# Performance work log

Hardware: AMD Instinct MI355X
Metric: run time of the kernel (lower is better)

The kernel has to match this reference:

```python
import jax, jax.numpy as jnp
import numpy as np

# ---- static config (matches init_kwargs) ----
B, S, D = 2, 4096, 1024          # batch, seq_len, dim_input
L, ST = 512, 64                  # segment_len, state_len
H = 8                            # num_heads
DK0, DV0, DK1, DV1 = 64, 64, 64, 64  # per-head key/value dims for 2 memory levels
DH = 4096                        # dim_hidden (MLP)
T = 2 * ST + L                   # tokens per segment block: [state, segment, state]


def setup_inputs() -> dict:
    key = jax.random.key(0)
    ks = jax.random.split(key, 18)
    f32 = jnp.float32
    def w(k, shape, fan_in):
        return (jax.random.normal(k, shape, dtype=f32) / np.float32(np.sqrt(fan_in)))
    return {
        "x": jax.random.normal(ks[0], (B, S, D), dtype=f32),
        "state_init": 0.02 * jax.random.normal(ks[1], (ST, D), dtype=f32),
        # level-0 projections: dim_input -> per-head (key/value)
        "Wq0": w(ks[2], (D, H, DK0), D),
        "Wk0": w(ks[3], (D, H, DK0), D),
        "Wv0": w(ks[4], (D, H, DV0), D),
        # level-1 projections: level-0 value dim -> per-head (key/value)
        "Wq1": w(ks[5], (H, DV0, DK1), DV0),
        "Wk1": w(ks[6], (H, DV0, DK1), DV0),
        "Wv1": w(ks[7], (H, DV0, DV1), DV0),
        # output projection back to dim_input
        "Wo": w(ks[8], (H, DV1, D), H * DV1),
        "bo": jnp.zeros((D,), f32),
        "g_attn": jnp.ones((D,), f32),
        "b_attn": jnp.zeros((D,), f32),
        "W1": w(ks[9], (D, DH), D),
        "b1": jnp.zeros((DH,), f32),
        "W2": w(ks[10], (DH, D), DH),
        "b2": jnp.zeros((D,), f32),
        "g_mlp": jnp.ones((D,), f32),
        "b_mlp": jnp.zeros((D,), f32),
    }


def _layernorm(x, g, b, eps=1e-5):
    mu = jnp.mean(x, axis=-1, keepdims=True)
    var = jnp.mean(jnp.square(x - mu), axis=-1, keepdims=True)
    return (x - mu) * jax.lax.rsqrt(var + eps) * g + b


def _rope(x, pos):
    # x: (B, H, T, dk); rotary embedding with base 10000
    dk = x.shape[-1]
    inv_freq = jnp.power(jnp.float32(10000.0), -jnp.arange(0, dk, 2, dtype=jnp.float32) / dk)
    ang = pos[:, None] * inv_freq[None, :]              # (T, dk/2)
    cos, sin = jnp.cos(ang), jnp.sin(ang)
    x1, x2 = x[..., 0::2], x[..., 1::2]
    r1 = x1 * cos - x2 * sin
    r2 = x1 * sin + x2 * cos
    return jnp.stack([r1, r2], axis=-1).reshape(x.shape)


def _attend(q, k, v, mask):
    # q,k: (B,H,T,dk); v: (B,H,T,dv); causal mask (T,T)
    scale = jnp.float32(1.0 / np.sqrt(q.shape[-1]))
    scores = jnp.einsum('bhqc,bhkc->bhqk', q, k) * scale
    scores = jnp.where(mask, scores, jnp.float32(-1e30))
    p = jax.nn.softmax(scores, axis=-1)
    return jnp.einsum('bhqk,bhkv->bhqv', p, v)


def _remmtas(x, state_init, Wq0, Wk0, Wv0, Wq1, Wk1, Wv1, Wo, bo):
    b, s, d = x.shape
    n_seg = s // L
    xs = x.reshape(b, n_seg, L, d).transpose(1, 0, 2, 3)   # (n_seg, B, L, D)
    mask = jnp.tril(jnp.ones((T, T), dtype=bool))
    pos = jnp.arange(T, dtype=jnp.float32)
    state0 = jnp.broadcast_to(state_init, (b, ST, d))

    def step(state, seg):
        toks = jnp.concatenate([state, seg, state], axis=1)      # (B, T, D)
        # memory level 0
        q0 = _rope(jnp.einsum('btd,dhk->bhtk', toks, Wq0), pos)
        k0 = _rope(jnp.einsum('btd,dhk->bhtk', toks, Wk0), pos)
        v0 = jnp.einsum('btd,dhv->bhtv', toks, Wv0)
        o0 = _attend(q0, k0, v0, mask)                           # (B,H,T,DV0)
        # memory level 1 (consumes level-0 values, per-head)
        q1 = _rope(jnp.einsum('bhtv,hvk->bhtk', o0, Wq1), pos)
        k1 = _rope(jnp.einsum('bhtv,hvk->bhtk', o0, Wk1), pos)
        v1 = jnp.einsum('bhtv,hvw->bhtw', o0, Wv1)
        o1 = _attend(q1, k1, v1, mask)                           # (B,H,T,DV1)
        out = jnp.einsum('bhtv,hvd->btd', o1, Wo) + bo           # (B,T,D)
        new_state = out[:, ST + L:]                              # trailing state tokens
        return new_state, out[:, ST:ST + L]                      # segment output

    _, outs = jax.lax.scan(step, state0, xs)                     # (n_seg, B, L, D)
    return outs.transpose(1, 0, 2, 3).reshape(b, s, d)


def reference(x, state_init, Wq0, Wk0, Wv0, Wq1, Wk1, Wv1, Wo, bo,
              g_attn, b_attn, W1, b1, W2, b2, g_mlp, b_mlp):
    a = _remmtas(x, state_init, Wq0, Wk0, Wv0, Wq1, Wk1, Wv1, Wo, bo)
    h = _layernorm(a + x, g_attn, b_attn)
    m = jax.nn.gelu(h @ W1 + b1, approximate=False) @ W2 + b2
    # note: second residual adds the ORIGINAL x, per the source code
    return _layernorm(m + x, g_mlp, b_mlp)
```

## Files before the change

kernel.cpp:

```cpp
#include <hip/hip_runtime.h>
#include <hip/hip_bf16.h>

typedef __hip_bfloat16 bf16;
typedef short bf16x8 __attribute__((ext_vector_type(8)));
typedef float f32x4 __attribute__((ext_vector_type(4)));

#define CB 2
#define CS 4096
#define CD 1024
#define CL 512
#define CST 64
#define CH 8
#define CT 640
#define CDH 4096
#define NSEG 8
#define LP 80

__device__ __forceinline__ float tof(float x) { return x; }
__device__ __forceinline__ float tof(bf16 x) { return __bfloat162float(x); }
__device__ __forceinline__ void storev(float* p, float v) { *p = v; }
__device__ __forceinline__ void storev(bf16* p, float v) { *p = __float2bfloat16(v); }

__device__ __forceinline__ float ldin(const void* p, size_t i, int f32w) {
    if (f32w) return ((const float*)p)[i];
    return __bfloat162float(((const bf16*)p)[i]);
}

__global__ void sniff_kernel(const void* x, int* flag) {
    if (threadIdx.x == 0 && blockIdx.x == 0) {
        const bf16* hb = (const bf16*)x;
        int plaus = 0;
        for (int i = 0; i < 256; ++i) {
            float v = __bfloat162float(hb[2 * i]);
            float a = fabsf(v);
            if (v == 0.f || (a > 1e-4f && a < 100.f)) ++plaus;
        }
        flag[0] = (plaus < 128) ? 1 : 0;
    }
}

__global__ __launch_bounds__(256) void transpose_kernel(
    const void* __restrict__ in, bf16* __restrict__ out, int R, int C,
    const int* __restrict__ flag)
{
    const int f32w = flag[0];
    __shared__ short t[64][72];
    int tid = threadIdx.x;
    int c0 = blockIdx.x * 64, r0 = blockIdx.y * 64;
    int cc = tid & 63, rr = tid >> 6;
#pragma unroll
    for (int i = 0; i < 16; ++i) {
        bf16 v = __float2bfloat16(ldin(in, (size_t)(r0 + rr + i * 4) * C + c0 + cc, f32w));
        t[rr + i * 4][cc] = *(short*)&v;
    }
    __syncthreads();
#pragma unroll
    for (int i = 0; i < 16; ++i)
        ((short*)out)[(size_t)(c0 + rr + i * 4) * R + r0 + cc] = t[cc][rr + i * 4];
}

__global__ __launch_bounds__(256) void transpose3_kernel(
    const void* __restrict__ in0, const void* __restrict__ in1, const void* __restrict__ in2,
    bf16* __restrict__ out0, bf16* __restrict__ out1, bf16* __restrict__ out2,
    const int* __restrict__ flag)
{
    const int f32w = flag[0];
    const void* in = (blockIdx.z == 0) ? in0 : (blockIdx.z == 1 ? in1 : in2);
    bf16* out = (blockIdx.z == 0) ? out0 : (blockIdx.z == 1 ? out1 : out2);
    const int R = CD, C = 512;
    __shared__ short t[64][72];
    int tid = threadIdx.x;
    int c0 = blockIdx.x * 64, r0 = blockIdx.y * 64;
    int cc = tid & 63, rr = tid >> 6;
#pragma unroll
    for (int i = 0; i < 16; ++i) {
        bf16 v = __float2bfloat16(ldin(in, (size_t)(r0 + rr + i * 4) * C + c0 + cc, f32w));
        t[rr + i * 4][cc] = *(short*)&v;
    }
    __syncthreads();
#pragma unroll
    for (int i = 0; i < 16; ++i)
        ((short*)out)[(size_t)(c0 + rr + i * 4) * R + r0 + cc] = t[cc][rr + i * 4];
}

__global__ __launch_bounds__(256) void transposeH_kernel(
    const void* __restrict__ Wq1, const void* __restrict__ Wk1, const void* __restrict__ Wv1,
    bf16* __restrict__ oq, bf16* __restrict__ ok, bf16* __restrict__ ov,
    const int* __restrict__ flag)
{
    const int f32w = flag[0];
    int which = blockIdx.x >> 3, hh = blockIdx.x & 7;
    const void* in = (which == 0) ? Wq1 : (which == 1) ? Wk1 : Wv1;
    bf16* out = (which == 0) ? oq : (which == 1) ? ok : ov;
    __shared__ short t[64][72];
    int tid = threadIdx.x;
    int cc = tid & 63, rr = tid >> 6;
    size_t base = (size_t)hh * 4096;
#pragma unroll
    for (int i = 0; i < 16; ++i) {
        bf16 v = __float2bfloat16(ldin(in, base + (size_t)(rr + i * 4) * 64 + cc, f32w));
        t[rr + i * 4][cc] = *(short*)&v;
    }
    __syncthreads();
#pragma unroll
    for (int i = 0; i < 16; ++i)
        ((short*)out)[base + (size_t)(rr + i * 4) * 64 + cc] = t[cc][rr + i * 4];
}

template <typename TC, int ACT, int OUTM, int ACCUM>
__global__ __launch_bounds__(256) void mfma_lds(
    const bf16* __restrict__ A,
    const bf16* __restrict__ Bt0, const bf16* __restrict__ Bt1, const bf16* __restrict__ Bt2,
    TC* __restrict__ C0, TC* __restrict__ C1, TC* __restrict__ C2,
    const void* __restrict__ bias, int boff,
    int M, int N, int K, int lda, int ldb, int seg,
    const int* __restrict__ flag)
{
    const int f32w = flag[0];
    const bf16* Bt = (blockIdx.z == 0) ? Bt0 : (blockIdx.z == 1 ? Bt1 : Bt2);
    TC* C = (blockIdx.z == 0) ? C0 : (blockIdx.z == 1 ? C1 : C2);

    __shared__ __align__(16) short As[128 * 64];
    __shared__ __align__(16) short Bs[128 * 64];

    const int tid = threadIdx.x;
    const int lane = tid & 63;
    const int w = tid >> 6;
    const int wm = w >> 1, wn = w & 1;
    const int bm = blockIdx.x * 128, bn = blockIdx.y * 128;

    f32x4 acc[4][4];
#pragma unroll
    for (int i = 0; i < 4; ++i)
#pragma unroll
        for (int j = 0; j < 4; ++j) acc[i][j] = (f32x4){0.f, 0.f, 0.f, 0.f};

    int srow[4], skc[4];
#pragma unroll
    for (int i = 0; i < 4; ++i) {
        int c = i * 256 + tid;
        srow[i] = c >> 3;
        skc[i] = (c & 7) * 8;
    }

    bf16x8 rA0[4], rB0[4], rA1[4], rB1[4];
#pragma unroll
    for (int i = 0; i < 4; ++i) {
        rA0[i] = *(const bf16x8*)(A + (size_t)(bm + srow[i]) * lda + skc[i]);
        rB0[i] = *(const bf16x8*)(Bt + (size_t)(bn + srow[i]) * ldb + skc[i]);
        rA1[i] = *(const bf16x8*)(A + (size_t)(bm + srow[i]) * lda + 64 + skc[i]);
        rB1[i] = *(const bf16x8*)(Bt + (size_t)(bn + srow[i]) * ldb + 64 + skc[i]);
    }

#define MFMA_PHASE                                                              \
    _Pragma("unroll")                                                           \
    for (int kh = 0; kh < 2; ++kh) {                                            \
        bf16x8 av[4], bv[4];                                                    \
        _Pragma("unroll")                                                       \
        for (int mi = 0; mi < 4; ++mi) {                                        \
            int r = wm * 64 + mi * 16 + (lane & 15);                            \
            int cl = kh * 4 + (lane >> 4);                                      \
            av[mi] = *(const bf16x8*)&As[r * 64 + cl * 8];                      \
        }                                                                       \
        _Pragma("unroll")                                                       \
        for (int nj = 0; nj < 4; ++nj) {                                        \
            int r = wn * 64 + nj * 16 + (lane & 15);                            \
            int cl = kh * 4 + (lane >> 4);                                      \
            bv[nj] = *(const bf16x8*)&Bs[r * 64 + cl * 8];                      \
        }                                                                       \
        _Pragma("unroll")                                                       \
        for (int mi = 0; mi < 4; ++mi)                                          \
            _Pragma("unroll")                                                   \
            for (int nj = 0; nj < 4; ++nj)                                      \
                acc[mi][nj] = __builtin_amdgcn_mfma_f32_16x16x32_bf16(          \
                    av[mi], bv[nj], acc[mi][nj], 0, 0, 0);                      \
    }

    for (int k0 = 0; k0 < K; k0 += 128) {
        __syncthreads();
#pragma unroll
        for (int i = 0; i < 4; ++i) {
            *(bf16x8*)&As[(size_t)(i * 256 + tid) * 8] = rA0[i];
            *(bf16x8*)&Bs[(size_t)(i * 256 + tid) * 8] = rB0[i];
        }
        if (k0 + 128 < K) {
            int kn = k0 + 128;
#pragma unroll
            for (int i = 0; i < 4; ++i) {
                rA0[i] = *(const bf16x8*)(A + (size_t)(bm + srow[i]) * lda + kn + skc[i]);
                rB0[i] = *(const bf16x8*)(Bt + (size_t)(bn + srow[i]) * ldb + kn + skc[i]);
            }
        }
        __syncthreads();
        MFMA_PHASE

        __syncthreads();
#pragma unroll
        for (int i = 0; i < 4; ++i) {
            *(bf16x8*)&As[(size_t)(i * 256 + tid) * 8] = rA1[i];
            *(bf16x8*)&Bs[(size_t)(i * 256 + tid) * 8] = rB1[i];
        }
        if (k0 + 192 < K) {
            int kn = k0 + 192;
#pragma unroll
            for (int i = 0; i < 4; ++i) {
                rA1[i] = *(const bf16x8*)(A + (size_t)(bm + srow[i]) * lda + kn + skc[i]);
                rB1[i] = *(const bf16x8*)(Bt + (size_t)(bn + srow[i]) * ldb + kn + skc[i]);
            }
        }
        __syncthreads();
        MFMA_PHASE
    }
#undef MFMA_PHASE

#pragma unroll
    for (int mi = 0; mi < 4; ++mi) {
#pragma unroll
        for (int nj = 0; nj < 4; ++nj) {
            int c = bn + wn * 64 + nj * 16 + (lane & 15);
            float bia = bias ? ldin(bias, boff + c, f32w) : 0.f;
#pragma unroll
            for (int r = 0; r < 4; ++r) {
                int row = bm + wm * 64 + mi * 16 + (lane >> 4) * 4 + r;
                float v = acc[mi][nj][r] + bia;
                if (ACT == 1) v = 0.5f * v * (1.0f + erff(v * 0.70710678118654752f));
                if (OUTM == 0) {
                    if (ACCUM) v += tof(C[(size_t)row * N + c]);
                    storev(C + (size_t)row * N + c, v);
                } else {
                    int bb2 = row / CT, t = row % CT;
                    if (t >= CST) {
                        if (t < CST + CL)
                            storev(C0 + ((size_t)bb2 * CS + (size_t)seg * CL + (t - CST)) * CD + c, v);
                        else
                            storev(C1 + ((size_t)bb2 * CST + (t - CST - CL)) * CD + c, v);
                    }
                }
            }
        }
    }
}

__global__ __launch_bounds__(256) void ropeV_kernel(
    bf16* __restrict__ q, bf16* __restrict__ k,
    const bf16* __restrict__ v, bf16* __restrict__ vt)
{
    int t0 = blockIdx.x * 64, hh = blockIdx.y, b = blockIdx.z;
    int tid = threadIdx.x;
    __shared__ short lt[64][72];
    int c = tid & 63;
    int r0 = tid >> 6;
    int ip = c >> 1;
    float inv = powf(10000.f, -(float)(2 * ip) / 64.f);
#pragma unroll
    for (int i = 0; i < 16; ++i) {
        int r = r0 + i * 4;
        int t = t0 + r;
        size_t idx = ((size_t)b * CT + t) * 512 + hh * 64 + c;
        float qv = tof(q[idx]);
        float kv = tof(k[idx]);
        float ang = (float)t * inv;
        float sn, cs;
        sincosf(ang, &sn, &cs);
        float qp = __shfl_xor(qv, 1);
        float kp = __shfl_xor(kv, 1);
        float rq, rk;
        if (c & 1) { rq = qp * sn + qv * cs; rk = kp * sn + kv * cs; }
        else       { rq = qv * cs - qp * sn; rk = kv * cs - kp * sn; }
        q[idx] = __float2bfloat16(rq);
        k[idx] = __float2bfloat16(rk);
        lt[r][c] = ((const short*)v)[idx];
    }
    __syncthreads();
#pragma unroll
    for (int i = 0; i < 16; ++i) {
        int c2 = r0 + i * 4;
        int r2 = c;
        ((short*)vt)[((size_t)(b * CH + hh) * 64 + c2) * CT + t0 + r2] = lt[r2][c2];
    }
}

template <int FUSE>
__global__ __launch_bounds__(256) void attn_mfma(
    const bf16* __restrict__ q, const bf16* __restrict__ k, const bf16* __restrict__ vt,
    bf16* __restrict__ o,
    int qsb, int qsh, int qst,
    int ksb, int ksh, int kst,
    int ob, int oh, int ot,
    const bf16* __restrict__ Wq1t, const bf16* __restrict__ Wk1t, const bf16* __restrict__ Wv1t,
    bf16* __restrict__ q1o, bf16* __restrict__ k1o, bf16* __restrict__ v1to)
{
    const int tid = threadIdx.x;
    const int lane = tid & 63;
    const int wrow = tid >> 6;
    const int hh = blockIdx.y, b = blockIdx.z;
    const int qbase = ((int)gridDim.x - 1 - (int)blockIdx.x) * 64;

    __shared__ __align__(16) short Qs[64 * LP];
    __shared__ __align__(16) short Ks[64 * LP];
    __shared__ __align__(16) short Vs[64 * LP];
    __shared__ __align__(16) short Ps[64 * LP];

    const size_t qb0 = (size_t)b * qsb + (size_t)hh * qsh;
    const size_t kb0 = (size_t)b * ksb + (size_t)hh * ksh;
    const size_t vtb = (size_t)(b * CH + hh) * 64 * CT;

    int srow[2], skc[2], soff[2];
#pragma unroll
    for (int i = 0; i < 2; ++i) {
        int c = i * 256 + tid;
        srow[i] = c >> 3;
        skc[i] = c & 7;
        soff[i] = srow[i] * LP + skc[i] * 8;
    }

    bf16x8 rQ[2], rK[2], rV[2];
#pragma unroll
    for (int i = 0; i < 2; ++i) {
        rQ[i] = *(const bf16x8*)(q + qb0 + (size_t)(qbase + srow[i]) * qst + skc[i] * 8);
        rK[i] = *(const bf16x8*)(k + kb0 + (size_t)srow[i] * kst + skc[i] * 8);
        rV[i] = *(const bf16x8*)(vt + vtb + (size_t)srow[i] * CT + skc[i] * 8);
    }

    float mrow[4], lrow[4];
    f32x4 oacc[4];
#pragma unroll
    for (int r = 0; r < 4; ++r) { mrow[r] = -1e30f; lrow[r] = 0.f; }
#pragma unroll
    for (int nd = 0; nd < 4; ++nd) oacc[nd] = (f32x4){0.f, 0.f, 0.f, 0.f};

    const int ntiles = qbase / 64 + 1;
    for (int ti = 0; ti < ntiles; ++ti) {
        __syncthreads();
        if (ti == 0) {
#pragma unroll
            for (int i = 0; i < 2; ++i) *(bf16x8*)&Qs[soff[i]] = rQ[i];
        }
#pragma unroll
        for (int i = 0; i < 2; ++i) {
            *(bf16x8*)&Ks[soff[i]] = rK[i];
            *(bf16x8*)&Vs[soff[i]] = rV[i];
        }
        if (ti + 1 < ntiles) {
            int j1 = (ti + 1) * 64;
#pragma unroll
            for (int i = 0; i < 2; ++i) {
                rK[i] = *(const bf16x8*)(k + kb0 + (size_t)(j1 + srow[i]) * kst + skc[i] * 8);
                rV[i] = *(const bf16x8*)(vt + vtb + (size_t)srow[i] * CT + j1 + skc[i] * 8);
            }
        }
        __syncthreads();

        f32x4 sacc[4];
#pragma unroll
        for (int nj = 0; nj < 4; ++nj) sacc[nj] = (f32x4){0.f, 0.f, 0.f, 0.f};
#pragma unroll
        for (int kh = 0; kh < 2; ++kh) {
            int cl = kh * 4 + (lane >> 4);
            bf16x8 av = *(const bf16x8*)&Qs[(wrow * 16 + (lane & 15)) * LP + cl * 8];
#pragma unroll
            for (int nj = 0; nj < 4; ++nj) {
                bf16x8 bv = *(const bf16x8*)&Ks[(nj * 16 + (lane & 15)) * LP + cl * 8];
                sacc[nj] = __builtin_amdgcn_mfma_f32_16x16x32_bf16(av, bv, sacc[nj], 0, 0, 0);
            }
        }

        const bool diag = (ti == ntiles - 1);
        float pm[4] = {-1e30f, -1e30f, -1e30f, -1e30f};
#pragma unroll
        for (int nj = 0; nj < 4; ++nj) {
            int col_l = nj * 16 + (lane & 15);
#pragma unroll
            for (int r = 0; r < 4; ++r) {
                int row_l = wrow * 16 + ((lane >> 4) << 2) + r;
                float s = (diag && col_l > row_l) ? -1e30f : sacc[nj][r] * 0.125f;
                sacc[nj][r] = s;
                pm[r] = fmaxf(pm[r], s);
            }
        }
#pragma unroll
        for (int msk = 1; msk < 16; msk <<= 1)
#pragma unroll
            for (int r = 0; r < 4; ++r) pm[r] = fmaxf(pm[r], __shfl_xor(pm[r], msk));

        float corr[4], rs[4] = {0.f, 0.f, 0.f, 0.f};
#pragma unroll
        for (int r = 0; r < 4; ++r) {
            float mn = fmaxf(mrow[r], pm[r]);
            corr[r] = __expf(mrow[r] - mn);
            mrow[r] = mn;
        }
#pragma unroll
        for (int nj = 0; nj < 4; ++nj)
#pragma unroll
            for (int r = 0; r < 4; ++r) {
                float p = __expf(sacc[nj][r] - mrow[r]);
                sacc[nj][r] = p;
                rs[r] += p;
            }
#pragma unroll
        for (int msk = 1; msk < 16; msk <<= 1)
#pragma unroll
            for (int r = 0; r < 4; ++r) rs[r] += __shfl_xor(rs[r], msk);
#pragma unroll
        for (int r = 0; r < 4; ++r) lrow[r] = lrow[r] * corr[r] + rs[r];
#pragma unroll
        for (int nd = 0; nd < 4; ++nd)
#pragma unroll
            for (int r = 0; r < 4; ++r) oacc[nd][r] *= corr[r];

#pragma unroll
        for (int nj = 0; nj < 4; ++nj)
#pragma unroll
            for (int r = 0; r < 4; ++r) {
                bf16 pb = __float2bfloat16(sacc[nj][r]);
                Ps[(wrow * 16 + ((lane >> 4) << 2) + r) * LP + nj * 16 + (lane & 15)] =
                    *(short*)&pb;
            }

#pragma unroll
        for (int kh = 0; kh < 2; ++kh) {
            int cl = kh * 4 + (lane >> 4);
            bf16x8 pa = *(const bf16x8*)&Ps[(wrow * 16 + (lane & 15)) * LP + cl * 8];
#pragma unroll
            for (int nd = 0; nd < 4; ++nd) {
                bf16x8 bv = *(const bf16x8*)&Vs[(nd * 16 + (lane & 15)) * LP + cl * 8];
                oacc[nd] = __builtin_amdgcn_mfma_f32_16x16x32_bf16(pa, bv, oacc[nd], 0, 0, 0);
            }
        }
    }

    if (FUSE == 0) {
#pragma unroll
        for (int nd = 0; nd < 4; ++nd) {
#pragma unroll
            for (int r = 0; r < 4; ++r) {
                int row_g = qbase + wrow * 16 + ((lane >> 4) << 2) + r;
                int col = nd * 16 + (lane & 15);
                storev(&o[(size_t)b * ob + (size_t)hh * oh + (size_t)row_g * ot + col],
                       oacc[nd][r] / lrow[r]);
            }
        }
    } else {
#pragma unroll
        for (int nd = 0; nd < 4; ++nd)
#pragma unroll
            for (int r = 0; r < 4; ++r) {
                int row_l = wrow * 16 + ((lane >> 4) << 2) + r;
                bf16 ob16 = __float2bfloat16(oacc[nd][r] / lrow[r]);
                Qs[row_l * LP + nd * 16 + (lane & 15)] = *(short*)&ob16;
            }
        __syncthreads();

        const size_t whb = (size_t)hh * 4096;
        f32x4 qa[4], ka[4], va[4];
#pragma unroll
        for (int nj = 0; nj < 4; ++nj) {
            qa[nj] = (f32x4){0.f, 0.f, 0.f, 0.f};
            ka[nj] = (f32x4){0.f, 0.f, 0.f, 0.f};
            va[nj] = (f32x4){0.f, 0.f, 0.f, 0.f};
        }
#pragma unroll
        for (int kh = 0; kh < 2; ++kh) {
            int cl = kh * 4 + (lane >> 4);
            bf16x8 av = *(const bf16x8*)&Qs[(wrow * 16 + (lane & 15)) * LP + cl * 8];
#pragma unroll
            for (int nj = 0; nj < 4; ++nj) {
                int rowb = nj * 16 + (lane & 15);
                bf16x8 bq = *(const bf16x8*)(Wq1t + whb + (size_t)rowb * 64 + cl * 8);
                bf16x8 bk = *(const bf16x8*)(Wk1t + whb + (size_t)rowb * 64 + cl * 8);
                bf16x8 bw = *(const bf16x8*)(Wv1t + whb + (size_t)rowb * 64 + cl * 8);
                qa[nj] = __builtin_amdgcn_mfma_f32_16x16x32_bf16(av, bq, qa[nj], 0, 0, 0);
                ka[nj] = __builtin_amdgcn_mfma_f32_16x16x32_bf16(av, bk, ka[nj], 0, 0, 0);
                va[nj] = __builtin_amdgcn_mfma_f32_16x16x32_bf16(av, bw, va[nj], 0, 0, 0);
            }
        }
        const size_t bh = (size_t)(b * CH + hh);
#pragma unroll
        for (int nj = 0; nj < 4; ++nj) {
            int col = nj * 16 + (lane & 15);
            int ip = col >> 1;
            float inv = powf(10000.f, -(float)(2 * ip) / 64.f);
#pragma unroll
            for (int r = 0; r < 4; ++r) {
                int row_l = wrow * 16 + ((lane >> 4) << 2) + r;
                int t = qbase + row_l;
                float ang = (float)t * inv;
                float sn, cs;
                sincosf(ang, &sn, &cs);
                float aq = qa[nj][r], ak = ka[nj][r];
                float pq = __shfl_xor(aq, 1);
                float pk = __shfl_xor(ak, 1);
                float rq, rk;
                if (col & 1) { rq = pq * sn + aq * cs; rk = pk * sn + ak * cs; }
                else         { rq = aq * cs - pq * sn; rk = ak * cs - pk * sn; }
                size_t roff = (bh * CT + t) * 64 + col;
                q1o[roff] = __float2bfloat16(rq);
                k1o[roff] = __float2bfloat16(rk);
                v1to[(bh * 64 + col) * CT + t] = __float2bfloat16(va[nj][r]);
            }
        }
    }
}

__global__ __launch_bounds__(256) void build_toks_kernel(
    const void* __restrict__ x, const float* __restrict__ state, bf16* __restrict__ toks,
    int seg, const int* __restrict__ flag)
{
    const int f32w = flag[0];
    int idx = blockIdx.x * 256 + threadIdx.x;
    int d = idx & (CD - 1);
    int t = (idx >> 10) % CT;
    int b = idx / (CT * CD);
    float v;
    if (t < CST) v = state[(b * CST + t) * CD + d];
    else if (t < CST + CL) v = ldin(x, ((size_t)b * CS + seg * CL + (t - CST)) * CD + d, f32w);
    else v = state[(b * CST + (t - CST - CL)) * CD + d];
    toks[idx] = __float2bfloat16(v);
}

__global__ __launch_bounds__(256) void init_state_kernel(
    const void* __restrict__ s0, float* __restrict__ state, const int* __restrict__ flag)
{
    const int f32w = flag[0];
    int idx = blockIdx.x * 256 + threadIdx.x;
    state[idx] = ldin(s0, idx % (CST * CD), f32w);
}

__global__ __launch_bounds__(256) void ln_kernel(
    const float* __restrict__ ra, const void* __restrict__ x,
    const void* __restrict__ g, const void* __restrict__ bb,
    void* __restrict__ outp, int out_ext, const int* __restrict__ flag)
{
    const int f32w = flag[0];
    int row = blockIdx.x;
    int tid = threadIdx.x;
    __shared__ float buf[CD];
    __shared__ float red[4];

    float s = 0.f;
    for (int c = tid; c < CD; c += 256) {
        float v = ra[(size_t)row * CD + c] + ldin(x, (size_t)row * CD + c, f32w);
        buf[c] = v;
        s += v;
    }
#pragma unroll
    for (int off = 32; off; off >>= 1) s += __shfl_xor(s, off);
    if ((tid & 63) == 0) red[tid >> 6] = s;
    __syncthreads();
    float mu = (red[0] + red[1] + red[2] + red[3]) * (1.f / CD);
    __syncthreads();

    float vs = 0.f;
    for (int c = tid; c < CD; c += 256) {
        float d0 = buf[c] - mu;
        vs += d0 * d0;
    }
#pragma unroll
    for (int off = 32; off; off >>= 1) vs += __shfl_xor(vs, off);
    if ((tid & 63) == 0) red[tid >> 6] = vs;
    __syncthreads();
    float var = (red[0] + red[1] + red[2] + red[3]) * (1.f / CD);
    float rs = rsqrtf(var + 1e-5f);

    for (int c = tid; c < CD; c += 256) {
        float y = (buf[c] - mu) * rs * ldin(g, c, f32w) + ldin(bb, c, f32w);
        size_t idx = (size_t)row * CD + c;
        if (!out_ext) {
            ((bf16*)outp)[idx] = __float2bfloat16(y);
        } else if (f32w) {
            ((float*)outp)[idx] = y;
        } else {
            ((bf16*)outp)[idx] = __float2bfloat16(y);
        }
    }
}

extern "C" void kernel_launch(void* const* d_in, const int* in_sizes, int n_in,
                              void* d_out, int out_size, void* d_ws, size_t ws_size,
                              hipStream_t stream)
{
    const void* x      = d_in[0];
    const void* s0     = d_in[1];
    const void* Wq0    = d_in[2];
    const void* Wk0    = d_in[3];
    const void* Wv0    = d_in[4];
    const void* Wq1    = d_in[5];
    const void* Wk1    = d_in[6];
    const void* Wv1    = d_in[7];
    const void* Wo     = d_in[8];
    const void* bo     = d_in[9];
    const void* g_attn = d_in[10];
    const void* b_attn = d_in[11];
    const void* W1     = d_in[12];
    const void* b1     = d_in[13];
    const void* W2     = d_in[14];
    const void* b2     = d_in[15];
    const void* g_mlp  = d_in[16];
    const void* b_mlp  = d_in[17];

    int* flag = (int*)d_ws;
    float* f = (float*)((char*)d_ws + 16);
    float* toks_slot = f; f += (size_t)CB * CT * CD;
    float* q0_slot = f;  f += (size_t)CB * CH * CT * 64;
    float* k0_slot = f;  f += (size_t)CB * CH * CT * 64;
    float* v0_slot = f;  f += (size_t)CB * CH * CT * 64;
    float* o0_slot = f;  f += (size_t)CB * CH * CT * 64;
    float* q1_slot = f;  f += (size_t)CB * CH * CT * 64;
    float* k1_slot = f;  f += (size_t)CB * CH * CT * 64;
    float* v1_slot = f;  f += (size_t)CB * CH * CT * 64;
    float* o1t_slot = f; f += (size_t)CB * CT * (CH * 64);
    float* seg_slot = f; f += (size_t)CB * CT * CD;
    float* state = f;   f += (size_t)CB * CST * CD;
    float* a = f;       f += (size_t)CB * CS * CD;
    bf16* h = (bf16*)f;
    bf16* tail = h + (size_t)CB * CS * CD;

    bf16* toks = (bf16*)toks_slot;
    bf16* q0b = (bf16*)q0_slot;
    bf16* k0b = (bf16*)k0_slot;
    bf16* v0b = (bf16*)v0_slot;
    bf16* v0t = (bf16*)o0_slot;
    bf16* q1b = (bf16*)q1_slot;
    bf16* k1b = (bf16*)k1_slot;
    bf16* v1t = (bf16*)v1_slot;
    bf16* o1t = (bf16*)o1t_slot;
    bf16* WtQ = h;
    bf16* WtK = WtQ + (size_t)512 * 1024;
    bf16* WtV = WtK + (size_t)512 * 1024;
    bf16* WtO = WtV + (size_t)512 * 1024;
    bf16* WtQ1 = WtO + (size_t)1024 * 512;
    bf16* WtK1 = WtQ1 + (size_t)8 * 4096;
    bf16* WtV1 = WtK1 + (size_t)8 * 4096;
    bf16* g1  = (bf16*)toks_slot;
    bf16* Wt1 = g1 + (size_t)CB * CS * CD;
    bf16* Wt2 = tail;

    sniff_kernel<<<1, 64, 0, stream>>>(x, flag);
    init_state_kernel<<<(CB * CST * CD) / 256, 256, 0, stream>>>(s0, state, flag);

    transpose3_kernel<<<dim3(8, 16, 3), 256, 0, stream>>>(
        Wq0, Wk0, Wv0, WtQ, WtK, WtV, flag);
    transpose_kernel<<<dim3(16, 8), 256, 0, stream>>>(Wo, WtO, 512, CD, flag);
    transposeH_kernel<<<24, 256, 0, stream>>>(Wq1, Wk1, Wv1, WtQ1, WtK1, WtV1, flag);

    for (int seg = 0; seg < NSEG; ++seg) {
        build_toks_kernel<<<(CB * CT * CD) / 256, 256, 0, stream>>>(x, state, toks, seg, flag);
        mfma_lds<bf16, 0, 0, 0><<<dim3(10, 4, 3), 256, 0, stream>>>(
            toks, WtQ, WtK, WtV, q0b, k0b, v0b, nullptr, 0,
            CB * CT, 512, CD, CD, CD, 0, flag);
        ropeV_kernel<<<dim3(CT / 64, CH, CB), 256, 0, stream>>>(q0b, k0b, v0b, v0t);
        attn_mfma<1><<<dim3(CT / 64, CH, CB), 256, 0, stream>>>(
            q0b, k0b, v0t, nullptr,
            CT * 512, 64, 512,
            CT * 512, 64, 512,
            0, 0, 0,
            WtQ1, WtK1, WtV1, q1b, k1b, v1t);
        attn_mfma<0><<<dim3(CT / 64, CH, CB), 256, 0, stream>>>(
            q1b, k1b, v1t, o1t,
            CH * CT * 64, CT * 64, 64,
            CH * CT * 64, CT * 64, 64,
            CT * 512, 64, 512,
            nullptr, nullptr, nullptr, nullptr, nullptr, nullptr);
        mfma_lds<float, 0, 1, 0><<<dim3(10, 8, 1), 256, 0, stream>>>(
            o1t, WtO, WtO, WtO, a, state, a, bo, 0,
            CB * CT, CD, 512, 512, 512, seg, flag);
    }

    ln_kernel<<<CB * CS, 256, 0, stream>>>(a, x, g_attn, b_attn, h, 0, flag);

    transpose_kernel<<<dim3(CDH / 64, CD / 64), 256, 0, stream>>>(W1, Wt1, CD, CDH, flag);
    transpose_kernel<<<dim3(CD / 64, CDH / 64), 256, 0, stream>>>(W2, Wt2, CDH, CD, flag);

    for (int c = 0; c < 4; ++c) {
        mfma_lds<bf16, 1, 0, 0><<<dim3(64, 8, 1), 256, 0, stream>>>(
            h, Wt1 + (size_t)c * 1024 * CD, Wt1, Wt1, g1, g1, g1,
            b1, c * 1024, CB * CS, 1024, CD, CD, CD, 0, flag);
        if (c == 0)
            mfma_lds<float, 0, 0, 0><<<dim3(64, 8, 1), 256, 0, stream>>>(
                g1, Wt2 + (size_t)c * 1024, Wt2, Wt2, a, a, a,
                b2, 0, CB * CS, CD, 1024, 1024, CDH, 0, flag);
        else
            mfma_lds<float, 0, 0, 1><<<dim3(64, 8, 1), 256, 0, stream>>>(
                g1, Wt2 + (size_t)c * 1024, Wt2, Wt2, a, a, a,
                nullptr, 0, CB * CS, CD, 1024, 1024, CDH, 0, flag);
    }
    ln_kernel<<<CB * CS, 256, 0, stream>>>(a, x, g_mlp, b_mlp, d_out, 1, flag);
}
```

Measured before the change: 1.214 ms.

## Defer segment output projection to one batched GEMM after the scan

Inside the segment loop, the level-1 attention now skips the leading state query block. It writes segment rows to a staging buffer and the trailing state rows to a small buffer. Only the 128 state rows get the per-segment output projection, which keeps the recurrent state chain intact. The projection of all segment tokens is then done in one large GEMM over B*S rows after the loop, replacing eight small under-occupied GEMMs. This adds a new output-mode branch and extra bf16 scratch buffers carved from the workspace.

```diff
diff --git a/kernel.cpp b/kernel.cpp
--- a/kernel.cpp
+++ b/kernel.cpp
@@ -228,13 +228,7 @@
                     if (ACCUM) v += tof(C[(size_t)row * N + c]);
                     storev(C + (size_t)row * N + c, v);
                 } else {
-                    int bb2 = row / CT, t = row % CT;
-                    if (t >= CST) {
-                        if (t < CST + CL)
-                            storev(C0 + ((size_t)bb2 * CS + (size_t)seg * CL + (t - CST)) * CD + c, v);
-                        else
-                            storev(C1 + ((size_t)bb2 * CST + (t - CST - CL)) * CD + c, v);
-                    }
+                    storev(C1 + (size_t)row * CD + c, v);
                 }
             }
         }
@@ -286,7 +280,7 @@
     bf16* __restrict__ o,
     int qsb, int qsh, int qst,
     int ksb, int ksh, int kst,
-    int ob, int oh, int ot,
+    int seg,
     const bf16* __restrict__ Wq1t, const bf16* __restrict__ Wk1t, const bf16* __restrict__ Wv1t,
     bf16* __restrict__ q1o, bf16* __restrict__ k1o, bf16* __restrict__ v1to)
 {
@@ -294,7 +288,8 @@
     const int lane = tid & 63;
     const int wrow = tid >> 6;
     const int hh = blockIdx.y, b = blockIdx.z;
-    const int qbase = ((int)gridDim.x - 1 - (int)blockIdx.x) * 64;
+    const int qbase = (FUSE ? ((int)gridDim.x - 1 - (int)blockIdx.x)
+                            : ((int)gridDim.x - (int)blockIdx.x)) * 64;
 
     __shared__ __align__(16) short Qs[64 * LP];
     __shared__ __align__(16) short Ks[64 * LP];
@@ -431,14 +426,18 @@
     }
 
     if (FUSE == 0) {
+        bf16* dst;
+        int rbase;
+        if (qbase == 576) { dst = q1o; rbase = b * 64 - 576; }
+        else              { dst = o;   rbase = (b * 8 + seg) * 512 - 64; }
 #pragma unroll
         for (int nd = 0; nd < 4; ++nd) {
 #pragma unroll
             for (int r = 0; r < 4; ++r) {
                 int row_g = qbase + wrow * 16 + ((lane >> 4) << 2) + r;
                 int col = nd * 16 + (lane & 15);
-                storev(&o[(size_t)b * ob + (size_t)hh * oh + (size_t)row_g * ot + col],
-                       oacc[nd][r] / lrow[r]);
+                dst[(size_t)(rbase + row_g) * 512 + hh * 64 + col] =
+                    __float2bfloat16(oacc[nd][r] / lrow[r]);
             }
         }
     } else {
@@ -624,7 +623,6 @@
     bf16* q1b = (bf16*)q1_slot;
     bf16* k1b = (bf16*)k1_slot;
     bf16* v1t = (bf16*)v1_slot;
-    bf16* o1t = (bf16*)o1t_slot;
     bf16* WtQ = h;
     bf16* WtK = WtQ + (size_t)512 * 1024;
     bf16* WtV = WtK + (size_t)512 * 1024;
@@ -632,6 +630,8 @@
     bf16* WtQ1 = WtO + (size_t)1024 * 512;
     bf16* WtK1 = WtQ1 + (size_t)8 * 4096;
     bf16* WtV1 = WtK1 + (size_t)8 * 4096;
+    bf16* o1mid = WtV1 + (size_t)8 * 4096;
+    bf16* o1s = o1mid + (size_t)CB * NSEG * 512 * 512;
     bf16* g1  = (bf16*)toks_slot;
     bf16* Wt1 = g1 + (size_t)CB * CS * CD;
     bf16* Wt2 = tail;
@@ -654,18 +654,22 @@
             q0b, k0b, v0t, nullptr,
             CT * 512, 64, 512,
             CT * 512, 64, 512,
-            0, 0, 0,
+            seg,
             WtQ1, WtK1, WtV1, q1b, k1b, v1t);
-        attn_mfma<0><<<dim3(CT / 64, CH, CB), 256, 0, stream>>>(
-            q1b, k1b, v1t, o1t,
+        attn_mfma<0><<<dim3(9, CH, CB), 256, 0, stream>>>(
+            q1b, k1b, v1t, o1mid,
             CH * CT * 64, CT * 64, 64,
             CH * CT * 64, CT * 64, 64,
-            CT * 512, 64, 512,
-            nullptr, nullptr, nullptr, nullptr, nullptr, nullptr);
-        mfma_lds<float, 0, 1, 0><<<dim3(10, 8, 1), 256, 0, stream>>>(
-            o1t, WtO, WtO, WtO, a, state, a, bo, 0,
-            CB * CT, CD, 512, 512, 512, seg, flag);
-    }
+            seg,
+            nullptr, nullptr, nullptr, o1s, nullptr, nullptr);
+        mfma_lds<float, 0, 2, 0><<<dim3(1, 8, 1), 256, 0, stream>>>(
+            o1s, WtO, WtO, WtO, a, state, a, bo, 0,
+            128, CD, 512, 512, 512, seg, flag);
+    }
+
+    mfma_lds<float, 0, 0, 0><<<dim3(64, 8, 1), 256, 0, stream>>>(
+        o1mid, WtO, WtO, WtO, a, a, a, bo, 0,
+        CB * CS, CD, 512, 512, 512, 0, flag);
 
     ln_kernel<<<CB * CS, 256, 0, stream>>>(a, x, g_attn, b_attn, h, 0, flag);
 
```

Measured after the change: 1.166 ms. 1.04x faster.
